# Kernel optimization log

Measured on AMD Instinct MI355X. Metric: run time of the kernel, lower is better.

The kernel has to match this reference:

```python
import jax, jax.numpy as jnp
import numpy as np
from jax import lax

B, C, H, W = 32, 3, 128, 128
S = 10             # max_segments
L = 200            # base_traj_length
TOTAL_LIMIT = 200  # traj_length (must equal L per original sample())
DOF = 2
HID = 2048
CONV_OUT = 512 * 6 * 6  # 128->126->63->61->30->28->14->12->6


def _conv(x, w, b):
    y = lax.conv_general_dilated(x, w, (1, 1), 'VALID', dimension_numbers=('NCHW', 'OIHW', 'NCHW'))
    return y + b[None, :, None, None]


def _pool_relu(x):
    return jax.nn.relu(lax.reduce_window(x, -jnp.inf, lax.max, (1, 1, 2, 2), (1, 1, 2, 2), 'VALID'))


def _rotate2d(y, y0, rot):
    # rotate points y (B,L,2) around per-batch center y0 (B,2) by rot (B,1,1) radians
    px, py = y[..., 0:1], y[..., 1:2]
    cx, cy = y0[:, 0][:, None, None], y0[:, 1][:, None, None]
    c, s = jnp.cos(rot), jnp.sin(rot)
    return jnp.concatenate([c * (px - cx) - s * (py - cy) + cx,
                            s * (px - cx) + c * (py - cy) + cy], axis=2)


def _sample(traj, ratio):
    b, T = traj.shape[0], traj.shape[1]
    f32 = traj.dtype
    seg_limit = jnp.ceil(ratio * TOTAL_LIMIT)  # (B,S)
    # redistribution: shave 1 off the (first) max segment while over budget.
    # original runs over_limit.max() iterations; over_limit <= S-1, extras are no-ops (still_over gate).
    for _ in range(S):
        max_val = seg_limit.max(axis=1)
        still_over = (seg_limit.sum(axis=1) != float(L)).astype(f32)
        reduced = jnp.ones((b,), f32)
        for j in range(S):
            mult = jnp.abs(jnp.sign(max_val - seg_limit[:, j]) - 1.0)
            seg_limit = seg_limit.at[:, j].add(-mult * reduced * still_over)
            reduced = jnp.clip(reduced - mult, 0.0)
    seg_ids = np.arange(T) // L
    # replicates original condition: i>0 and cur_segment_idx != floor(i - 1/L)  (note: i - 1/L, as written)
    forces = np.array([(i > 0) and (seg_ids[i] != int(np.floor(i - 1.0 / L))) for i in range(T)])
    di0 = jnp.floor((L - 1.0) / seg_limit[:, 0:1])
    init = (di0, jnp.zeros((b, 1), f32), jnp.zeros((b, 1), f32), jnp.zeros((b, S), f32))

    def step(state, inp):
        di, last_idx, n_tot, seg_cnt = state
        i_f, seg, force = inp
        lim = lax.dynamic_index_in_dim(seg_limit, seg, axis=1, keepdims=True)  # (B,1)
        cnt = lax.dynamic_index_in_dim(seg_cnt, seg, axis=1, keepdims=True)    # (B,1)
        new_di = jnp.floor((L - 1.0 - (last_idx - seg.astype(f32) * L)) / (lim - cnt))
        di = jnp.where(force | (di < new_di), new_di, di)
        chk = (jnp.sign(jnp.clip(TOTAL_LIMIT - n_tot, 0.0))
               * (cnt < lim).astype(f32)
               * (i_f - last_idx == di).astype(f32))
        last_idx = jnp.maximum(last_idx, i_f * chk)
        seg_cnt = lax.dynamic_update_index_in_dim(seg_cnt, (cnt + chk)[:, 0], seg, axis=1)
        return (di, last_idx, n_tot + chk, seg_cnt), chk[:, 0]

    xs = (jnp.arange(T, dtype=f32), jnp.asarray(seg_ids, jnp.int32), jnp.asarray(forces))
    _, mask_t = lax.scan(step, init, xs)
    mask = mask_t.T > 0  # (B,T) velocity mask; exactly TOTAL_LIMIT true per row
    idx = jnp.argsort(jnp.where(mask, 0, 1), axis=1)[:, :TOTAL_LIMIT]  # stable sort -> ordered true positions
    return jnp.take_along_axis(traj, idx[:, :, None], axis=1)


def _forward(x, w1, b1, w2, b2, w3, b3, w4, b4, fcw1, fcb1, fcw2, fcb2,
             wi, bi, ws, bs, wr, br, base_traj):
    h = _pool_relu(_conv(x, w1, b1))
    h = _pool_relu(_conv(h, w2, b2))
    h = _pool_relu(_conv(h, w3, b3))
    h = _pool_relu(_conv(h, w4, b4))
    feat = h.reshape(h.shape[0], -1)  # (B, CONV_OUT)
    z = jnp.tanh(feat @ fcw1.T + fcb1)
    z = z @ fcw2.T + fcb2             # dropout == identity (eval mode)
    init_pos = z @ wi.T + bi                                   # (B,DOF)
    seg_mod = (z @ ws.T + bs).reshape(z.shape[0], S, DOF + 1)  # (B,S,DOF+1)
    ratio = jax.nn.softmax(z @ wr.T + br, axis=1)              # (B,S)
    last_pos = init_pos[:, None, :]
    starts, segs = [last_pos], []
    for i in range(S):
        scaling = seg_mod[:, i, :-1]
        rot = jnp.tanh(seg_mod[:, i, -1])[:, None, None] * 3.14
        m = base_traj * scaling[:, None, :]
        m = _rotate2d(m, m[:, 0, :], rot)
        m = last_pos + m
        last_pos = m[:, -1:, :]
        starts.append(last_pos)
        segs.append(m)
    traj = jnp.concatenate(segs, axis=1)             # (B,S*L,DOF) unsampled
    seg_start_end = jnp.concatenate(starts, axis=1)  # (B,S+1,DOF)
    sampled = _sample(traj, ratio)                   # (B,TOTAL_LIMIT,DOF)
    return sampled, seg_start_end, ratio, traj


def setup_inputs():
    key = jax.random.key(0)
    ks = jax.random.split(key, 12)
    n = lambda k, s, sc: jax.random.normal(k, s, jnp.float32) * sc
    t = jnp.linspace(0.0, 1.0, L)
    base_traj = jnp.stack([t, jnp.sin(t * jnp.pi)], axis=-1)[None]  # (1,L,2)
    return {
        'x': n(ks[0], (B, C, H, W), 1.0),
        'w1': n(ks[1], (64, C, 3, 3), 0.05), 'b1': jnp.zeros((64,), jnp.float32),
        'w2': n(ks[2], (128, 64, 3, 3), 0.05), 'b2': jnp.zeros((128,), jnp.float32),
        'w3': n(ks[3], (256, 128, 3, 3), 0.05), 'b3': jnp.zeros((256,), jnp.float32),
        'w4': n(ks[4], (512, 256, 3, 3), 0.05), 'b4': jnp.zeros((512,), jnp.float32),
        'fcw1': n(ks[5], (HID, CONV_OUT), 0.01), 'fcb1': jnp.zeros((HID,), jnp.float32),
        'fcw2': n(ks[6], (HID, HID), 0.02), 'fcb2': jnp.zeros((HID,), jnp.float32),
        'wi': n(ks[7], (DOF, HID), 0.02), 'bi': jnp.zeros((DOF,), jnp.float32),
        'ws': n(ks[8], (S * (DOF + 1), HID), 0.02), 'bs': jnp.zeros((S * (DOF + 1),), jnp.float32),
        'wr': n(ks[9], (S, HID), 0.05), 'br': jnp.zeros((S,), jnp.float32),
        'base_traj': base_traj,
    }


def reference(x, w1, b1, w2, b2, w3, b3, w4, b4, fcw1, fcb1, fcw2, fcb2,
              wi, bi, ws, bs, wr, br, base_traj):
    return _forward(x, w1, b1, w2, b2, w3, b3, w4, b4, fcw1, fcb1, fcw2, fcb2,
                    wi, bi, ws, bs, wr, br, base_traj)
```

## Files before the change

kernel.cpp:

```cpp
#include <hip/hip_runtime.h>

__global__ __launch_bounds__(256)
void conv1_lds(const float* __restrict__ in, const float* __restrict__ wt,
               const float* __restrict__ bias, float* __restrict__ out)
{
    __shared__ float sh[3][34][34];
    int bx = blockIdx.x;
    int tile = bx & 15;
    int cg   = (bx >> 4) & 7;
    int b    = bx >> 7;
    int tr = tile >> 2, tc = tile & 3;
    int tid = threadIdx.x;
    int ty = tid >> 4, tx = tid & 15;
    int R0 = 32 * tr, C0 = 32 * tc;

    for (int t = tid; t < 3 * 34 * 34; t += 256) {
        int ci = t / 1156;
        int rem = t - ci * 1156;
        int rr = rem / 34, cc = rem - rr * 34;
        int gr = R0 + rr; if (gr > 127) gr = 127;
        int gc = C0 + cc; if (gc > 127) gc = 127;
        sh[ci][rr][cc] = in[(((size_t)b * 3 + ci) * 128 + gr) * 128 + gc];
    }
    __syncthreads();

    float acc[8][2][2] = {};
    int co0 = cg * 8;
#pragma unroll
    for (int ci = 0; ci < 3; ++ci) {
        float p[4][4];
#pragma unroll
        for (int r = 0; r < 4; ++r) {
            const float2* pr = reinterpret_cast<const float2*>(&sh[ci][2 * ty + r][2 * tx]);
            float2 a = pr[0], c2 = pr[1];
            p[r][0] = a.x; p[r][1] = a.y; p[r][2] = c2.x; p[r][3] = c2.y;
        }
#pragma unroll
        for (int j = 0; j < 8; ++j) {
            const float* wj = wt + ((size_t)(co0 + j) * 3 + ci) * 9;
#pragma unroll
            for (int kh = 0; kh < 3; ++kh)
#pragma unroll
                for (int kw = 0; kw < 3; ++kw) {
                    float wv = wj[kh * 3 + kw];
#pragma unroll
                    for (int dy = 0; dy < 2; ++dy)
#pragma unroll
                        for (int dx = 0; dx < 2; ++dx)
                            acc[j][dy][dx] = fmaf(wv, p[dy + kh][dx + kw], acc[j][dy][dx]);
                }
        }
    }
    int py = 16 * tr + ty, px = 16 * tc + tx;
    if (py < 63 && px < 63) {
#pragma unroll
        for (int j = 0; j < 8; ++j) {
            float v = fmaxf(fmaxf(acc[j][0][0], acc[j][0][1]),
                            fmaxf(acc[j][1][0], acc[j][1][1])) + bias[co0 + j];
            out[(((size_t)b * 64 + co0 + j) * 63 + py) * 63 + px] = fmaxf(v, 0.f);
        }
    }
}

template<int CIN, int DIM, int POOL, int COUT, int TILES_R, int TILES_C>
__global__ __launch_bounds__(256)
void conv_v9(const float* __restrict__ in, const float* __restrict__ wt,
             const float* __restrict__ bias, float* __restrict__ out)
{
    __shared__ __align__(16) float in_sh[2][648];
    __shared__ __align__(16) float w_sh[2][384];

    constexpr int NT  = TILES_R * TILES_C;
    constexpr int NCG = COUT / 32;
    int bx = blockIdx.x;
    int tile = bx % NT;
    int cg   = (bx / NT) % NCG;
    int b    = bx / (NT * NCG);
    int rt = tile / TILES_C, ct = tile % TILES_C;
    int tid = threadIdx.x;
    int co_l = tid & 15;
    int sp   = tid >> 4;
    int ty = sp >> 2, tx = sp & 3;
    int R0 = 16 * rt, C0 = 32 * ct;

    int gofs[3], lofs[3];
#pragma unroll
    for (int j = 0; j < 3; ++j) {
        int t = tid + 256 * j; if (t > 611) t = 611;
        int rr = t / 34, cc = t - rr * 34;
        int gr = R0 + rr; if (gr > DIM - 1) gr = DIM - 1;
        int gc = C0 + cc; if (gc > DIM - 1) gc = DIM - 1;
        gofs[j] = gr * DIM + gc;
        lofs[j] = rr * 36 + cc;
    }
    int wgofs[2], wlofs[2];
#pragma unroll
    for (int j = 0; j < 2; ++j) {
        int t = tid + 256 * j; if (t > 287) t = 287;
        int c = t / 9, k = t - c * 9;
        wgofs[j] = (cg * 32 + c) * CIN * 9 + k;
        wlofs[j] = c * 12 + k;
    }
    bool wv1 = (tid < 32);

    const float* gci = in + (size_t)b * CIN * DIM * DIM;
    const float* wci = wt;

    float acc[2][4][8] = {};
    float sr[3], wr[2];

#pragma unroll
    for (int j = 0; j < 3; ++j) sr[j] = gci[gofs[j]];
    wr[0] = wci[wgofs[0]];
    wr[1] = wci[wgofs[1]];
#pragma unroll
    for (int j = 0; j < 3; ++j) { int t = tid + 256 * j; if (t < 612) in_sh[0][lofs[j]] = sr[j]; }
    w_sh[0][wlofs[0]] = wr[0];
    if (wv1) w_sh[0][wlofs[1]] = wr[1];
    __syncthreads();

    for (int ci = 0; ci < CIN; ++ci) {
        int p = ci & 1;
        if (ci < CIN - 1) {
            const float* gn = gci + (size_t)(ci + 1) * DIM * DIM;
            const float* wn = wci + (size_t)(ci + 1) * 9;
#pragma unroll
            for (int j = 0; j < 3; ++j) sr[j] = gn[gofs[j]];
            wr[0] = wn[wgofs[0]];
            wr[1] = wn[wgofs[1]];
        }
        float w[2][9];
#pragma unroll
        for (int h = 0; h < 2; ++h)
#pragma unroll
            for (int k = 0; k < 9; ++k)
                w[h][k] = w_sh[p][(co_l + 16 * h) * 12 + k];
        const float* rb = in_sh[p] + 8 * tx;
#pragma unroll
        for (int r = 0; r < 6; ++r) {
            const float* rp = rb + (4 * ty + r) * 36;
            float4 a = *reinterpret_cast<const float4*>(rp);
            float4 b4 = *reinterpret_cast<const float4*>(rp + 4);
            float2 c2 = *reinterpret_cast<const float2*>(rp + 8);
            float row[10];
            row[0] = a.x;  row[1] = a.y;  row[2] = a.z;  row[3] = a.w;
            row[4] = b4.x; row[5] = b4.y; row[6] = b4.z; row[7] = b4.w;
            row[8] = c2.x; row[9] = c2.y;
#pragma unroll
            for (int y = 0; y < 4; ++y) {
                if (y < r - 2 || y > r) continue;
                int kh = r - y;
#pragma unroll
                for (int kw = 0; kw < 3; ++kw) {
                    float w0 = w[0][kh * 3 + kw];
                    float w1 = w[1][kh * 3 + kw];
#pragma unroll
                    for (int x = 0; x < 8; ++x) {
                        acc[0][y][x] = fmaf(w0, row[x + kw], acc[0][y][x]);
                        acc[1][y][x] = fmaf(w1, row[x + kw], acc[1][y][x]);
                    }
                }
            }
        }
        if (ci < CIN - 1) {
#pragma unroll
            for (int j = 0; j < 3; ++j) { int t = tid + 256 * j; if (t < 612) in_sh[p ^ 1][lofs[j]] = sr[j]; }
            w_sh[p ^ 1][wlofs[0]] = wr[0];
            if (wv1) w_sh[p ^ 1][wlofs[1]] = wr[1];
        }
        __syncthreads();
    }

#pragma unroll
    for (int h = 0; h < 2; ++h) {
        int co = cg * 32 + co_l + 16 * h;
        float bz = bias[co];
#pragma unroll
        for (int dy = 0; dy < 2; ++dy) {
            int py = 8 * rt + 2 * ty + dy;
#pragma unroll
            for (int dx = 0; dx < 4; ++dx) {
                int px = 16 * ct + 4 * tx + dx;
                if (py < POOL && px < POOL) {
                    float v = fmaxf(fmaxf(acc[h][2 * dy][2 * dx],     acc[h][2 * dy][2 * dx + 1]),
                                    fmaxf(acc[h][2 * dy + 1][2 * dx], acc[h][2 * dy + 1][2 * dx + 1]));
                    out[(((size_t)b * COUT + co) * POOL + py) * POOL + px] = fmaxf(v + bz, 0.f);
                }
            }
        }
    }
}

template<int CIN, int DIM, int POOL, int COUT, int TILES_R, int TILES_C>
__global__ __launch_bounds__(256)
void conv_v7(const float* __restrict__ in, const float* __restrict__ wt,
             const float* __restrict__ bias, float* __restrict__ out)
{
    __shared__ __align__(16) float sh[4 * 18 * 36];
    __shared__ float wsh[16 * 37];

    constexpr int NT  = TILES_R * TILES_C;
    constexpr int NCG = COUT / 16;
    int bx = blockIdx.x;
    int tile = bx % NT;
    int cg   = (bx / NT) % NCG;
    int b    = bx / (NT * NCG);
    int rt = tile / TILES_C, ct = tile % TILES_C;
    int tid = threadIdx.x;
    int co_l = tid & 15;
    int sp   = tid >> 4;
    int ty = sp >> 2, tx = sp & 3;
    int co = cg * 16 + co_l;
    int R0 = 16 * rt, C0 = 32 * ct;

    int gofs[10], lofs[10];
#pragma unroll
    for (int j = 0; j < 10; ++j) {
        int t = tid + 256 * j; if (t > 2447) t = 2447;
        int ci = t / 612;
        int rem = t - ci * 612;
        int rr = rem / 34, cc = rem - rr * 34;
        int gr = R0 + rr; if (gr > DIM - 1) gr = DIM - 1;
        int gc = C0 + cc; if (gc > DIM - 1) gc = DIM - 1;
        gofs[j] = ci * DIM * DIM + gr * DIM + gc;
        lofs[j] = ci * 648 + rr * 36 + cc;
    }
    int wgofs[3], wlofs[3];
#pragma unroll
    for (int j = 0; j < 3; ++j) {
        int t = tid + 256 * j; if (t > 575) t = 575;
        int c = t / 36, q = t - c * 36;
        wgofs[j] = (cg * 16 + c) * CIN * 9 + q;
        wlofs[j] = c * 37 + q;
    }

    const float* gbase = in + (size_t)b * CIN * DIM * DIM;

    float acc[4][8] = {};
    float sr[10], wr[3];

#pragma unroll
    for (int j = 0; j < 10; ++j) sr[j] = gbase[gofs[j]];
#pragma unroll
    for (int j = 0; j < 3; ++j) wr[j] = wt[wgofs[j]];

    constexpr int ITERS = CIN / 4;
    for (int it = 0; it < ITERS; ++it) {
#pragma unroll
        for (int j = 0; j < 10; ++j) sh[lofs[j]] = sr[j];
#pragma unroll
        for (int j = 0; j < 3; ++j) wsh[wlofs[j]] = wr[j];
        __syncthreads();
        if (it < ITERS - 1) {
            const float* gn = gbase + (size_t)(it + 1) * 4 * DIM * DIM;
#pragma unroll
            for (int j = 0; j < 10; ++j) sr[j] = gn[gofs[j]];
            const float* wn = wt + (it + 1) * 36;
#pragma unroll
            for (int j = 0; j < 3; ++j) wr[j] = wn[wgofs[j]];
        }
#pragma unroll
        for (int ci = 0; ci < 4; ++ci) {
            float w[9];
#pragma unroll
            for (int k = 0; k < 9; ++k) w[k] = wsh[co_l * 37 + ci * 9 + k];
            const float* rb = sh + ci * 648 + 8 * tx;
#pragma unroll
            for (int r = 0; r < 6; ++r) {
                const float* rp = rb + (4 * ty + r) * 36;
                float4 a = *reinterpret_cast<const float4*>(rp);
                float4 b4 = *reinterpret_cast<const float4*>(rp + 4);
                float2 c2 = *reinterpret_cast<const float2*>(rp + 8);
                float row[10];
                row[0] = a.x;  row[1] = a.y;  row[2] = a.z;  row[3] = a.w;
                row[4] = b4.x; row[5] = b4.y; row[6] = b4.z; row[7] = b4.w;
                row[8] = c2.x; row[9] = c2.y;
#pragma unroll
                for (int y = 0; y < 4; ++y) {
                    if (y < r - 2 || y > r) continue;
                    int kh = r - y;
#pragma unroll
                    for (int kw = 0; kw < 3; ++kw) {
                        float wv = w[kh * 3 + kw];
#pragma unroll
                        for (int x = 0; x < 8; ++x)
                            acc[y][x] = fmaf(wv, row[x + kw], acc[y][x]);
                    }
                }
            }
        }
        __syncthreads();
    }
    float bz = bias[co];
#pragma unroll
    for (int dy = 0; dy < 2; ++dy) {
        int py = 8 * rt + 2 * ty + dy;
#pragma unroll
        for (int dx = 0; dx < 4; ++dx) {
            int px = 16 * ct + 4 * tx + dx;
            if (py < POOL && px < POOL) {
                float v = fmaxf(fmaxf(acc[2 * dy][2 * dx],     acc[2 * dy][2 * dx + 1]),
                                fmaxf(acc[2 * dy + 1][2 * dx], acc[2 * dy + 1][2 * dx + 1]));
                out[(((size_t)b * COUT + co) * POOL + py) * POOL + px] = fmaxf(v + bz, 0.f);
            }
        }
    }
}

__global__ __launch_bounds__(256)
void conv4_v3(const float* __restrict__ in, const float* __restrict__ wt,
              const float* __restrict__ bias, float* __restrict__ out)
{
    __shared__ __align__(16) float smem[4032 + 4 * 16 * 37];
    float* in_sh = smem;
    float* w_sh  = smem + 4032;
    float* red   = smem;

    int bx = blockIdx.x;
    int cg = bx & 31;
    int b  = bx >> 5;
    int tid = threadIdx.x;
    int h   = tid >> 6;
    int r6  = tid & 63;
    int cog = r6 >> 3;
    int sub = r6 & 7;
    int R = 3 * (sub >> 1), C = 6 * (sub & 1);

    float acc[2][3][6] = {};
    float sin_r[13];
    float sw_r[9];

    const size_t in_b = (size_t)b * 256 * 196;

#pragma unroll
    for (int j = 0; j < 13; ++j) {
        int g = tid + 256 * j;
        if (g < 3136) {
            int hh = g / 784, rem = g - hh * 784;
            int ci = rem / 196, r2 = rem - ci * 196;
            sin_r[j] = in[in_b + (size_t)(hh * 64 + ci) * 196 + r2];
        }
    }
#pragma unroll
    for (int j = 0; j < 9; ++j) {
        int g = tid + 256 * j;
        int hh = g / 576, rem = g - hh * 576;
        int co = rem / 36, q = rem - co * 36;
        sw_r[j] = wt[(size_t)(cg * 16 + co) * 2304 + (size_t)(hh * 64) * 9 + q];
    }

    for (int it = 0; it < 16; ++it) {
#pragma unroll
        for (int j = 0; j < 13; ++j) {
            int g = tid + 256 * j;
            if (g < 3136) {
                int hh = g / 784, rem = g - hh * 784;
                int ci = rem / 196, r2 = rem - ci * 196;
                int rr = r2 / 14, cc = r2 - rr * 14;
                in_sh[((hh * 4 + ci) * 14 + rr) * 18 + cc] = sin_r[j];
            }
        }
#pragma unroll
        for (int j = 0; j < 9; ++j) {
            int g = tid + 256 * j;
            int hh = g / 576, rem = g - hh * 576;
            int co = rem / 36, q = rem - co * 36;
            w_sh[(hh * 16 + co) * 37 + q] = sw_r[j];
        }
        __syncthreads();
        if (it < 15) {
            int k0n = (it + 1) * 4;
#pragma unroll
            for (int j = 0; j < 13; ++j) {
                int g = tid + 256 * j;
                if (g < 3136) {
                    int hh = g / 784, rem = g - hh * 784;
                    int ci = rem / 196, r2 = rem - ci * 196;
                    sin_r[j] = in[in_b + (size_t)(hh * 64 + k0n + ci) * 196 + r2];
                }
            }
#pragma unroll
            for (int j = 0; j < 9; ++j) {
                int g = tid + 256 * j;
                int hh = g / 576, rem = g - hh * 576;
                int co = rem / 36, q = rem - co * 36;
                sw_r[j] = wt[(size_t)(cg * 16 + co) * 2304 + (size_t)(hh * 64 + k0n) * 9 + q];
            }
        }
#pragma unroll
        for (int ci = 0; ci < 4; ++ci) {
            float w[2][9];
#pragma unroll
            for (int c = 0; c < 2; ++c)
#pragma unroll
                for (int k = 0; k < 9; ++k)
                    w[c][k] = w_sh[(h * 16 + 2 * cog + c) * 37 + ci * 9 + k];
            const float* rowbase = in_sh + ((h * 4 + ci) * 14) * 18;
#pragma unroll
            for (int r = 0; r < 5; ++r) {
                float row[8];
                const float2* pr = reinterpret_cast<const float2*>(rowbase + (size_t)(R + r) * 18 + C);
                float2 a0 = pr[0], a1 = pr[1], a2 = pr[2], a3 = pr[3];
                row[0] = a0.x; row[1] = a0.y; row[2] = a1.x; row[3] = a1.y;
                row[4] = a2.x; row[5] = a2.y; row[6] = a3.x; row[7] = a3.y;
#pragma unroll
                for (int y = 0; y < 3; ++y) {
                    if (y < r - 2 || y > r) continue;
                    int kh = r - y;
#pragma unroll
                    for (int c = 0; c < 2; ++c)
#pragma unroll
                        for (int kw = 0; kw < 3; ++kw) {
                            float wv = w[c][kh * 3 + kw];
#pragma unroll
                            for (int x = 0; x < 6; ++x)
                                acc[c][y][x] = fmaf(wv, row[x + kw], acc[c][y][x]);
                        }
                }
            }
        }
        __syncthreads();
    }
#pragma unroll
    for (int hh = 0; hh < 4; ++hh) {
        if (h == hh) {
#pragma unroll
            for (int c = 0; c < 2; ++c)
#pragma unroll
                for (int y = 0; y < 3; ++y)
#pragma unroll
                    for (int x = 0; x < 6; ++x) {
                        float* dst = &red[((2 * cog + c) * 12 + R + y) * 13 + C + x];
                        if (hh == 0) *dst = acc[c][y][x];
                        else         *dst += acc[c][y][x];
                    }
        }
        __syncthreads();
    }
    for (int t = tid; t < 576; t += 256) {
        int co = t / 36, rem = t - co * 36;
        int pr = rem / 6, pc = rem - pr * 6;
        const float* rp = &red[(co * 12 + 2 * pr) * 13 + 2 * pc];
        float v = fmaxf(fmaxf(rp[0], rp[1]), fmaxf(rp[13], rp[14]));
        v += bias[cg * 16 + co];
        out[(((size_t)b * 512 + cg * 16 + co) * 6 + pr) * 6 + pc] = fmaxf(v, 0.f);
    }
}

__global__ __launch_bounds__(1024)
void fc_big(const float* __restrict__ X, const float* __restrict__ W,
            const float* __restrict__ bias, float* __restrict__ Y,
            int K, int N, int act)
{
    __shared__ float red[32][32][8];
    int o0 = blockIdx.x * 8;
    int s = threadIdx.x & 31;
    int b = threadIdx.x >> 5;
    int K4 = K >> 2;
    const float4* X4 = reinterpret_cast<const float4*>(X) + (size_t)b * K4;
    const float4* W4 = reinterpret_cast<const float4*>(W);

    float acc[8] = {};
    for (int k4 = s; k4 < K4; k4 += 32) {
        float4 xv = X4[k4];
#pragma unroll
        for (int o = 0; o < 8; ++o) {
            float4 wv = W4[(size_t)(o0 + o) * K4 + k4];
            acc[o] = fmaf(xv.x, wv.x,
                     fmaf(xv.y, wv.y,
                     fmaf(xv.z, wv.z,
                     fmaf(xv.w, wv.w, acc[o]))));
        }
    }
#pragma unroll
    for (int o = 0; o < 8; ++o) red[b][s][o] = acc[o];
    __syncthreads();
    if (threadIdx.x < 256) {
        int bb = threadIdx.x >> 3, oo = threadIdx.x & 7;
        float v = bias[o0 + oo];
#pragma unroll 8
        for (int ss = 0; ss < 32; ++ss) v += red[bb][ss][oo];
        if (act) v = tanhf(v);
        Y[(size_t)bb * N + o0 + oo] = v;
    }
}

__global__ __launch_bounds__(256)
void fc_two(const float* __restrict__ X, const float* __restrict__ W,
            const float* __restrict__ bias, float* __restrict__ Y,
            int K, int N, int act)
{
    int o0 = blockIdx.x * 2;
    int tid = threadIdx.x;
    const float* w0 = W + (size_t)o0 * K;
    const float* w1 = w0 + K;
    float a0[32], a1[32];
#pragma unroll
    for (int b = 0; b < 32; ++b) { a0[b] = 0.f; a1[b] = 0.f; }

    for (int k = tid; k < K; k += 256) {
        float wv0 = w0[k], wv1 = w1[k];
#pragma unroll
        for (int b = 0; b < 32; ++b) {
            float xv = X[(size_t)b * K + k];
            a0[b] = fmaf(wv0, xv, a0[b]);
            a1[b] = fmaf(wv1, xv, a1[b]);
        }
    }
    __shared__ float part[2][4][32];
    int lane = tid & 63, wv = tid >> 6;
#pragma unroll
    for (int b = 0; b < 32; ++b) {
        float s0 = a0[b], s1 = a1[b];
#pragma unroll
        for (int off = 32; off >= 1; off >>= 1) {
            s0 += __shfl_down(s0, off);
            s1 += __shfl_down(s1, off);
        }
        if (lane == 0) { part[0][wv][b] = s0; part[1][wv][b] = s1; }
    }
    __syncthreads();
    if (tid < 64) {
        int j = tid >> 5, b = tid & 31;
        float s = part[j][0][b] + part[j][1][b] + part[j][2][b] + part[j][3][b] + bias[o0 + j];
        if (act) s = tanhf(s);
        Y[(size_t)b * N + o0 + j] = s;
    }
}

__global__ __launch_bounds__(64)
void post_kernel(const float* __restrict__ logits, float* __restrict__ ratio_out,
                 float* __restrict__ sl_out)
{
    int b = threadIdx.x;
    if (b >= 32) return;
    float lg[10];
#pragma unroll
    for (int j = 0; j < 10; ++j) lg[j] = logits[b * 10 + j];
    float mx = lg[0];
#pragma unroll
    for (int j = 1; j < 10; ++j) mx = fmaxf(mx, lg[j]);
    float e[10]; float ssum = 0.f;
#pragma unroll
    for (int j = 0; j < 10; ++j) { e[j] = expf(lg[j] - mx); ssum += e[j]; }
    float sl[10];
#pragma unroll
    for (int j = 0; j < 10; ++j) {
        float r = e[j] / ssum;
        ratio_out[b * 10 + j] = r;
        sl[j] = ceilf(r * 200.f);
    }
#pragma unroll
    for (int it = 0; it < 10; ++it) {
        float s = 0.f, mx2 = sl[0];
#pragma unroll
        for (int j = 0; j < 10; ++j) { s += sl[j]; mx2 = fmaxf(mx2, sl[j]); }
        float over = (s != 200.f) ? 1.f : 0.f;
        float reduced = 1.f;
#pragma unroll
        for (int j = 0; j < 10; ++j) {
            float mult = (sl[j] == mx2) ? 1.f : 0.f;
            sl[j] -= mult * reduced * over;
            reduced = fmaxf(reduced - mult, 0.f);
        }
    }
#pragma unroll
    for (int j = 0; j < 10; ++j) sl_out[b * 10 + j] = sl[j];
}

__global__ __launch_bounds__(256)
void traj_kernel(const float* __restrict__ base, const float* __restrict__ ipos,
                 const float* __restrict__ sm, float* __restrict__ out_traj,
                 float* __restrict__ out_starts)
{
    int b = blockIdx.x;
    int j = threadIdx.x;
    float bx0 = base[0], by0 = base[1];
    float bxL = base[398], byL = base[399];
    float bx = 0.f, by = 0.f;
    if (j < 200) { bx = base[2 * j]; by = base[2 * j + 1]; }
    float curx = ipos[b * 2 + 0], cury = ipos[b * 2 + 1];
    if (j == 0) { out_starts[b * 22 + 0] = curx; out_starts[b * 22 + 1] = cury; }
#pragma unroll
    for (int i = 0; i < 10; ++i) {
        float sx  = sm[b * 30 + i * 3 + 0];
        float sy  = sm[b * 30 + i * 3 + 1];
        float rot = tanhf(sm[b * 30 + i * 3 + 2]) * 3.14f;
        float c = cosf(rot), s = sinf(rot);
        float cx = bx0 * sx, cy = by0 * sy;
        if (j < 200) {
            float px = bx * sx, py = by * sy;
            float rx = c * (px - cx) - s * (py - cy) + cx;
            float ry = s * (px - cx) + c * (py - cy) + cy;
            size_t o = ((size_t)b * 2000 + i * 200 + j) * 2;
            out_traj[o + 0] = curx + rx;
            out_traj[o + 1] = cury + ry;
        }
        float pxL = bxL * sx, pyL = byL * sy;
        float exL = c * (pxL - cx) - s * (pyL - cy) + cx;
        float eyL = s * (pxL - cx) + c * (pyL - cy) + cy;
        curx += exL; cury += eyL;
        if (j == 0) {
            out_starts[b * 22 + (i + 1) * 2 + 0] = curx;
            out_starts[b * 22 + (i + 1) * 2 + 1] = cury;
        }
    }
}

__global__ __launch_bounds__(64)
void sample_kernel(const float* __restrict__ sl_in, const float* __restrict__ traj,
                   float* __restrict__ samp_out)
{
    __shared__ unsigned int maskb[32][63];
    __shared__ float ssl[32][10];
    int tid = threadIdx.x;
    for (int t = tid; t < 32 * 63; t += 64) ((unsigned int*)maskb)[t] = 0u;
    for (int t = tid; t < 32 * 10; t += 64) ((float*)ssl)[t] = sl_in[t];
    __syncthreads();
    if (tid >= 32) return;
    int b = tid;
    const float* tb = traj + (size_t)b * 4000;
    float* sp = samp_out + (size_t)b * 400;
    int out_n = 0;
    float last = 0.f, ntot = 0.f;
    float lim0 = ssl[b][0];
    float di = floorf(199.f / lim0);
    float ct0 = 0.f;
    if ((ntot < 200.f) && (ct0 < lim0) && (0.f - last == di)) {
        ntot += 1.f; ct0 += 1.f;
        maskb[b][0] |= 1u;
        sp[out_n * 2] = tb[0]; sp[out_n * 2 + 1] = tb[1]; ++out_n;
    }
    {
        float ndi = floorf((199.f - last) / (lim0 - ct0));
        if (di < ndi) di = ndi;
        if ((ntot < 200.f) && (ct0 < lim0) && (1.f - last == di)) {
            last = 1.f; ntot += 1.f; ct0 += 1.f;
            maskb[b][0] |= 2u;
            sp[out_n * 2] = tb[2]; sp[out_n * 2 + 1] = tb[3]; ++out_n;
        }
    }
    for (int seg = 0; seg < 10; ++seg) {
        float lim = ssl[b][seg];
        float ct = (seg == 0) ? ct0 : 0.f;
        float segbase = 200.f * seg;
        float segend = segbase + 199.f;
        float pos = (seg == 0) ? 2.f : segbase;
        float ndi = floorf((199.f - (last - segbase)) / (lim - ct));
        while ((ntot < 200.f) && (ct < lim)) {
            float fi = last + ndi;
            if (!(fi >= pos && fi <= segend)) break;
            int i = (int)fi;
            last = fi; ntot += 1.f; ct += 1.f;
            maskb[b][i >> 5] |= (1u << (i & 31));
            sp[out_n * 2] = tb[2 * i]; sp[out_n * 2 + 1] = tb[2 * i + 1]; ++out_n;
            pos = fi + 1.f;
            ndi = floorf((199.f - (last - segbase)) / (lim - ct));
        }
    }
    for (int i = 0; i < 2000 && out_n < 200; ++i) {
        if (!((maskb[b][i >> 5] >> (i & 31)) & 1u)) {
            sp[out_n * 2] = tb[2 * i]; sp[out_n * 2 + 1] = tb[2 * i + 1]; ++out_n;
        }
    }
}

extern "C" void kernel_launch(void* const* d_in, const int* in_sizes, int n_in,
                              void* d_out, int out_size, void* d_ws, size_t ws_size,
                              hipStream_t stream)
{
    const float* x    = (const float*)d_in[0];
    const float* w1   = (const float*)d_in[1];
    const float* b1   = (const float*)d_in[2];
    const float* w2   = (const float*)d_in[3];
    const float* b2   = (const float*)d_in[4];
    const float* w3   = (const float*)d_in[5];
    const float* b3   = (const float*)d_in[6];
    const float* w4   = (const float*)d_in[7];
    const float* b4   = (const float*)d_in[8];
    const float* fcw1 = (const float*)d_in[9];
    const float* fcb1 = (const float*)d_in[10];
    const float* fcw2 = (const float*)d_in[11];
    const float* fcb2 = (const float*)d_in[12];
    const float* wi   = (const float*)d_in[13];
    const float* bi   = (const float*)d_in[14];
    const float* wsw  = (const float*)d_in[15];
    const float* bs   = (const float*)d_in[16];
    const float* wr   = (const float*)d_in[17];
    const float* br   = (const float*)d_in[18];
    const float* base = (const float*)d_in[19];

    float* out = (float*)d_out;
    float* ws  = (float*)d_ws;

    float* p1   = ws + 0;
    float* p2   = ws + 8128512;
    float* p3   = ws + 0;
    float* feat = ws + 8128512;
    float* z1   = ws + 0;
    float* z2   = ws + 65536;
    float* ipos = ws + 131072;
    float* smod = ws + 131136;
    float* rlog = ws + 132096;
    float* slim = ws + 132416;

    float* out_samp   = out;
    float* out_starts = out + 12800;
    float* out_ratio  = out + 13504;
    float* out_traj   = out + 13824;

    conv1_lds<<<4096, 256, 0, stream>>>(x, w1, b1, p1);
    conv_v9<64, 63, 30, 128, 4, 2><<<1024, 256, 0, stream>>>(p1, w2, b2, p2);
    conv_v7<128, 30, 14, 256, 2, 1><<<1024, 256, 0, stream>>>(p2, w3, b3, p3);
    conv4_v3<<<1024, 256, 0, stream>>>(p3, w4, b4, feat);

    fc_big<<<256, 1024, 0, stream>>>(feat, fcw1, fcb1, z1, 18432, 2048, 1);
    fc_big<<<256, 1024, 0, stream>>>(z1, fcw2, fcb2, z2, 2048, 2048, 0);

    fc_two<<<1, 256, 0, stream>>>(z2, wi, bi, ipos, 2048, 2, 0);
    fc_two<<<15, 256, 0, stream>>>(z2, wsw, bs, smod, 2048, 30, 0);
    fc_two<<<5, 256, 0, stream>>>(z2, wr, br, rlog, 2048, 10, 0);

    post_kernel<<<1, 64, 0, stream>>>(rlog, out_ratio, slim);
    traj_kernel<<<32, 256, 0, stream>>>(base, ipos, smod, out_traj, out_starts);
    sample_kernel<<<1, 64, 0, stream>>>(slim, out_traj, out_samp);
}
```

Baseline: 987.1 us.

## Replace conv3 kernel with 32-channel register tiling and double-buffered LDS

The templated conv3 kernel is replaced by a specialised kernel. Each thread now computes two output channels instead of one, so every input value loaded from LDS feeds twice as many FMAs. Input and weight tiles are double-buffered in shared memory, so one barrier per iteration suffices and global loads overlap compute. Grid shrinks from 1024 to 512 blocks with more accumulator registers per thread, which risks lower occupancy and fewer waves.

```diff
diff --git a/kernel.cpp b/kernel.cpp
--- a/kernel.cpp
+++ b/kernel.cpp
@@ -191,117 +191,132 @@
     }
 }
 
-template<int CIN, int DIM, int POOL, int COUT, int TILES_R, int TILES_C>
 __global__ __launch_bounds__(256)
-void conv_v7(const float* __restrict__ in, const float* __restrict__ wt,
-             const float* __restrict__ bias, float* __restrict__ out)
-{
-    __shared__ __align__(16) float sh[4 * 18 * 36];
-    __shared__ float wsh[16 * 37];
-
-    constexpr int NT  = TILES_R * TILES_C;
-    constexpr int NCG = COUT / 16;
+void conv3_v11(const float* __restrict__ in, const float* __restrict__ wt,
+               const float* __restrict__ bias, float* __restrict__ out)
+{
+    __shared__ __align__(16) float in_sh[2][1296];
+    __shared__ __align__(16) float w_sh[2][768];
+
     int bx = blockIdx.x;
-    int tile = bx % NT;
-    int cg   = (bx / NT) % NCG;
-    int b    = bx / (NT * NCG);
-    int rt = tile / TILES_C, ct = tile % TILES_C;
+    int tile = bx & 1;
+    int cg   = (bx >> 1) & 7;
+    int b    = bx >> 4;
+    int rt = tile;
     int tid = threadIdx.x;
     int co_l = tid & 15;
     int sp   = tid >> 4;
     int ty = sp >> 2, tx = sp & 3;
-    int co = cg * 16 + co_l;
-    int R0 = 16 * rt, C0 = 32 * ct;
-
-    int gofs[10], lofs[10];
-#pragma unroll
-    for (int j = 0; j < 10; ++j) {
-        int t = tid + 256 * j; if (t > 2447) t = 2447;
-        int ci = t / 612;
-        int rem = t - ci * 612;
+    int R0 = 16 * rt;
+
+    int gofs[5], lofs[5];
+#pragma unroll
+    for (int j = 0; j < 5; ++j) {
+        int t = tid + 256 * j; if (t > 1223) t = 1223;
+        int c2 = t / 612;
+        int rem = t - c2 * 612;
         int rr = rem / 34, cc = rem - rr * 34;
-        int gr = R0 + rr; if (gr > DIM - 1) gr = DIM - 1;
-        int gc = C0 + cc; if (gc > DIM - 1) gc = DIM - 1;
-        gofs[j] = ci * DIM * DIM + gr * DIM + gc;
-        lofs[j] = ci * 648 + rr * 36 + cc;
+        int gr = R0 + rr; if (gr > 29) gr = 29;
+        int gc = cc;      if (gc > 29) gc = 29;
+        gofs[j] = c2 * 900 + gr * 30 + gc;
+        lofs[j] = c2 * 648 + rr * 36 + cc;
     }
     int wgofs[3], wlofs[3];
 #pragma unroll
     for (int j = 0; j < 3; ++j) {
         int t = tid + 256 * j; if (t > 575) t = 575;
-        int c = t / 36, q = t - c * 36;
-        wgofs[j] = (cg * 16 + c) * CIN * 9 + q;
-        wlofs[j] = c * 37 + q;
-    }
-
-    const float* gbase = in + (size_t)b * CIN * DIM * DIM;
-
-    float acc[4][8] = {};
-    float sr[10], wr[3];
-
-#pragma unroll
-    for (int j = 0; j < 10; ++j) sr[j] = gbase[gofs[j]];
+        int c2 = t / 288;
+        int rem = t - c2 * 288;
+        int c = rem / 9, k = rem - c * 9;
+        wgofs[j] = (cg * 32 + c) * 1152 + c2 * 9 + k;
+        wlofs[j] = c2 * 384 + c * 12 + k;
+    }
+
+    const float* gci = in + (size_t)b * 128 * 900;
+
+    float acc[2][4][8] = {};
+    float sr[5], wr[3];
+
+#pragma unroll
+    for (int j = 0; j < 5; ++j) sr[j] = gci[gofs[j]];
 #pragma unroll
     for (int j = 0; j < 3; ++j) wr[j] = wt[wgofs[j]];
-
-    constexpr int ITERS = CIN / 4;
-    for (int it = 0; it < ITERS; ++it) {
-#pragma unroll
-        for (int j = 0; j < 10; ++j) sh[lofs[j]] = sr[j];
-#pragma unroll
-        for (int j = 0; j < 3; ++j) wsh[wlofs[j]] = wr[j];
-        __syncthreads();
-        if (it < ITERS - 1) {
-            const float* gn = gbase + (size_t)(it + 1) * 4 * DIM * DIM;
-#pragma unroll
-            for (int j = 0; j < 10; ++j) sr[j] = gn[gofs[j]];
-            const float* wn = wt + (it + 1) * 36;
+#pragma unroll
+    for (int j = 0; j < 5; ++j) { int t = tid + 256 * j; if (t < 1224) in_sh[0][lofs[j]] = sr[j]; }
+#pragma unroll
+    for (int j = 0; j < 3; ++j) { int t = tid + 256 * j; if (t < 576) w_sh[0][wlofs[j]] = wr[j]; }
+    __syncthreads();
+
+    for (int it = 0; it < 64; ++it) {
+        int p = it & 1;
+        if (it < 63) {
+            const float* gn = gci + (size_t)(it + 1) * 1800;
+            const float* wn = wt + (size_t)(it + 1) * 18;
+#pragma unroll
+            for (int j = 0; j < 5; ++j) sr[j] = gn[gofs[j]];
 #pragma unroll
             for (int j = 0; j < 3; ++j) wr[j] = wn[wgofs[j]];
         }
 #pragma unroll
-        for (int ci = 0; ci < 4; ++ci) {
-            float w[9];
-#pragma unroll
-            for (int k = 0; k < 9; ++k) w[k] = wsh[co_l * 37 + ci * 9 + k];
-            const float* rb = sh + ci * 648 + 8 * tx;
+        for (int c2 = 0; c2 < 2; ++c2) {
+            float w[2][9];
+#pragma unroll
+            for (int h = 0; h < 2; ++h)
+#pragma unroll
+                for (int k = 0; k < 9; ++k)
+                    w[h][k] = w_sh[p][c2 * 384 + (co_l + 16 * h) * 12 + k];
+            const float* rb = in_sh[p] + c2 * 648 + 8 * tx;
 #pragma unroll
             for (int r = 0; r < 6; ++r) {
                 const float* rp = rb + (4 * ty + r) * 36;
                 float4 a = *reinterpret_cast<const float4*>(rp);
                 float4 b4 = *reinterpret_cast<const float4*>(rp + 4);
-                float2 c2 = *reinterpret_cast<const float2*>(rp + 8);
+                float2 c2v = *reinterpret_cast<const float2*>(rp + 8);
                 float row[10];
                 row[0] = a.x;  row[1] = a.y;  row[2] = a.z;  row[3] = a.w;
                 row[4] = b4.x; row[5] = b4.y; row[6] = b4.z; row[7] = b4.w;
-                row[8] = c2.x; row[9] = c2.y;
+                row[8] = c2v.x; row[9] = c2v.y;
 #pragma unroll
                 for (int y = 0; y < 4; ++y) {
                     if (y < r - 2 || y > r) continue;
                     int kh = r - y;
 #pragma unroll
                     for (int kw = 0; kw < 3; ++kw) {
-                        float wv = w[kh * 3 + kw];
-#pragma unroll
-                        for (int x = 0; x < 8; ++x)
-                            acc[y][x] = fmaf(wv, row[x + kw], acc[y][x]);
+                        float w0 = w[0][kh * 3 + kw];
+                        float w1 = w[1][kh * 3 + kw];
+#pragma unroll
+                        for (int x = 0; x < 8; ++x) {
+                            acc[0][y][x] = fmaf(w0, row[x + kw], acc[0][y][x]);
+                            acc[1][y][x] = fmaf(w1, row[x + kw], acc[1][y][x]);
+                        }
                     }
                 }
             }
         }
+        if (it < 63) {
+#pragma unroll
+            for (int j = 0; j < 5; ++j) { int t = tid + 256 * j; if (t < 1224) in_sh[p ^ 1][lofs[j]] = sr[j]; }
+#pragma unroll
+            for (int j = 0; j < 3; ++j) { int t = tid + 256 * j; if (t < 576) w_sh[p ^ 1][wlofs[j]] = wr[j]; }
+        }
         __syncthreads();
     }
-    float bz = bias[co];
-#pragma unroll
-    for (int dy = 0; dy < 2; ++dy) {
-        int py = 8 * rt + 2 * ty + dy;
-#pragma unroll
-        for (int dx = 0; dx < 4; ++dx) {
-            int px = 16 * ct + 4 * tx + dx;
-            if (py < POOL && px < POOL) {
-                float v = fmaxf(fmaxf(acc[2 * dy][2 * dx],     acc[2 * dy][2 * dx + 1]),
-                                fmaxf(acc[2 * dy + 1][2 * dx], acc[2 * dy + 1][2 * dx + 1]));
-                out[(((size_t)b * COUT + co) * POOL + py) * POOL + px] = fmaxf(v + bz, 0.f);
+
+#pragma unroll
+    for (int h = 0; h < 2; ++h) {
+        int co = cg * 32 + co_l + 16 * h;
+        float bz = bias[co];
+#pragma unroll
+        for (int dy = 0; dy < 2; ++dy) {
+            int py = 8 * rt + 2 * ty + dy;
+#pragma unroll
+            for (int dx = 0; dx < 4; ++dx) {
+                int px = 4 * tx + dx;
+                if (py < 14 && px < 14) {
+                    float v = fmaxf(fmaxf(acc[h][2 * dy][2 * dx],     acc[h][2 * dy][2 * dx + 1]),
+                                    fmaxf(acc[h][2 * dy + 1][2 * dx], acc[h][2 * dy + 1][2 * dx + 1]));
+                    out[(((size_t)b * 256 + co) * 14 + py) * 14 + px] = fmaxf(v + bz, 0.f);
+                }
             }
         }
     }
@@ -711,7 +726,7 @@
 
     conv1_lds<<<4096, 256, 0, stream>>>(x, w1, b1, p1);
     conv_v9<64, 63, 30, 128, 4, 2><<<1024, 256, 0, stream>>>(p1, w2, b2, p2);
-    conv_v7<128, 30, 14, 256, 2, 1><<<1024, 256, 0, stream>>>(p2, w3, b3, p3);
+    conv3_v11<<<512, 256, 0, stream>>>(p2, w3, b3, p3);
     conv4_v3<<<1024, 256, 0, stream>>>(p3, w4, b4, feat);
 
     fc_big<<<256, 1024, 0, stream>>>(feat, fcw1, fcb1, z1, 18432, 2048, 1);
```

Result: slower. 1.044 ms (+5.7%).
